# Kernel optimization log

Hardware: AMD Instinct MI355X
Metric: run time of the kernel (lower is better)

## Reference

```python
import jax, jax.numpy as jnp
import numpy as np
import math

B, T, IN_DIM = 2, 2048, 512
D, NH, MULT, N_LAYER = 512, 8, 4, 3
N = D * MULT // NH  # per-head latent dim = 256
OUT_DIM = 512
THETA = 2 ** 16


def get_freqs(n):
    t = jnp.arange(n, dtype=jnp.float32)
    q = jnp.floor(t / 2.0) * 2.0  # quantize(q=2)
    return 1.0 / (THETA ** (q / n)) / (2.0 * math.pi)


def ln(x, eps=1e-5):
    mu = jnp.mean(x, axis=-1, keepdims=True)
    var = jnp.var(x, axis=-1, keepdims=True)
    return (x - mu) * jax.lax.rsqrt(var + eps)


def rope(phases, v):
    # phases: [T, N] broadcastable to v [B, nh, T, N]
    p = (phases % 1.0) * (2.0 * math.pi)
    pc, ps = jnp.cos(p), jnp.sin(p)
    # interleave rotate: out[..., 2i] = -v[..., 2i+1], out[..., 2i+1] = v[..., 2i]
    v_rot = jnp.stack((-v[..., 1::2], v[..., ::2]), axis=-1).reshape(v.shape)
    return v * pc + v_rot * ps


def setup_inputs() -> dict:
    key = jax.random.key(0)
    ks = jax.random.split(key, 8)
    std = 0.02
    return {
        "x": jax.random.normal(ks[0], (B, T, IN_DIM), dtype=jnp.float32),
        "w_in": jax.random.normal(ks[1], (IN_DIM, D), dtype=jnp.float32) * std,
        "b_in": jnp.zeros((D,), dtype=jnp.float32),
        "encoder": jax.random.normal(ks[2], (NH, D, N), dtype=jnp.float32) * std,
        "encoder_v": jax.random.normal(ks[3], (NH, D, N), dtype=jnp.float32) * std,
        "decoder": jax.random.normal(ks[4], (NH * N, D), dtype=jnp.float32) * std,
        "head_w": jax.random.normal(ks[5], (D, OUT_DIM), dtype=jnp.float32) * std,
        "head_b": jnp.zeros((OUT_DIM,), dtype=jnp.float32),
    }


def reference(x, w_in, b_in, encoder, encoder_v, decoder, head_w, head_b):
    freqs = get_freqs(N)  # [N]
    t_idx = jnp.arange(T, dtype=jnp.float32)
    phases = t_idx[:, None] * freqs[None, :]  # [T, N]
    # strict lower-triangular causal mask (tril diagonal=-1)
    mask = (jnp.arange(T)[:, None] > jnp.arange(T)[None, :])  # [T, T]
    dec = decoder.reshape(NH, N, D)

    xs = ln(x @ w_in + b_in)  # [B, T, D]
    for _ in range(N_LAYER):
        x_res = xs
        x_sparse = jax.nn.relu(jnp.einsum('btd,hdn->bhtn', xs, encoder))  # [B,nh,T,N]
        QR = rope(phases, x_sparse)
        scores = jnp.einsum('bhtn,bhsn->bhts', QR, QR)
        scores = jnp.where(mask, scores, 0.0)
        yKV = jnp.einsum('bhts,bsd->bhtd', scores, xs)  # V = x (head-broadcast)
        yKV = ln(yKV)
        y_sparse = jax.nn.relu(jnp.einsum('bhtd,hdn->bhtn', yKV, encoder_v))
        xy_sparse = x_sparse * y_sparse  # dropout p=0 -> identity
        yMLP = jnp.einsum('bhtn,hnd->btd', xy_sparse, dec)
        xs = ln(x_res + ln(yMLP))
    logits = xs @ head_w + head_b
    return logits
```

## Files before the change

kernel.cpp:

```cpp
#include <hip/hip_runtime.h>
#include <math.h>

constexpr int B_  = 2;
constexpr int T_  = 2048;
constexpr int D_  = 512;
constexpr int NH_ = 8;
constexpr int NL_ = 256;
constexpr int HN_ = NH_ * NL_;
constexpr int BT_ = B_ * T_;

typedef __bf16 v8bf __attribute__((ext_vector_type(8)));
typedef float  v4f  __attribute__((ext_vector_type(4)));
typedef unsigned short us8 __attribute__((ext_vector_type(8)));
typedef unsigned short us4 __attribute__((ext_vector_type(4)));

__device__ inline unsigned short f2b(float f) {
    union { float f; unsigned u; } v{f};
    unsigned r = v.u + 0x7FFF + ((v.u >> 16) & 1);
    return (unsigned short)(r >> 16);
}
__device__ inline float b2f(unsigned short u) {
    union { unsigned u; float f; } v{(unsigned)u << 16};
    return v.f;
}

__device__ __forceinline__ void g2l16(const void* g, void* l) {
    __builtin_amdgcn_global_load_lds(
        (const __attribute__((address_space(1))) void*)g,
        (__attribute__((address_space(3))) void*)l, 16, 0, 0);
}

#define TILE_IDS                                              \
    int tid = threadIdx.x;                                    \
    int lane = tid & 63, wid = tid >> 6;                      \
    int wm = (wid & 1) * 64, wn = (wid >> 1) * 64;            \
    int ln16 = lane & 15, q = lane >> 4;                      \
    int srl = lane >> 2, scl = (lane & 3) * 8;                \
    (void)wm; (void)wn;

#define T128_STAGE(Ab, lda, Bb, ldb, k0, buf)                 \
    _Pragma("unroll")                                         \
    for (int ci = 0; ci < 4; ++ci) {                          \
        int c = wid * 4 + ci;                                 \
        if (c < 8) {                                          \
            int r = c * 16 + srl;                             \
            g2l16(Ab + (long)r * lda + (k0) + scl,            \
                  (char*)As[buf] + c * 1024);                 \
        } else {                                              \
            int r = (c - 8) * 16 + srl;                       \
            g2l16(Bb + (long)r * ldb + (k0) + scl,            \
                  (char*)Bs[buf] + (c - 8) * 1024);           \
        }                                                     \
    }

#define TILE_MFMA(Asx, Bsx)                                   \
    {                                                         \
        v8bf af[4], bfr[4];                                   \
        _Pragma("unroll")                                     \
        for (int r = 0; r < 4; ++r)                           \
            af[r] = *(const v8bf*)&Asx[wm + r * 16 + ln16][q * 8]; \
        _Pragma("unroll")                                     \
        for (int c = 0; c < 4; ++c)                           \
            bfr[c] = *(const v8bf*)&Bsx[wn + c * 16 + ln16][q * 8]; \
        _Pragma("unroll")                                     \
        for (int r = 0; r < 4; ++r)                           \
            _Pragma("unroll")                                 \
            for (int c = 0; c < 4; ++c)                       \
                acc[r][c] = __builtin_amdgcn_mfma_f32_16x16x32_bf16( \
                    af[r], bfr[c], acc[r][c], 0, 0, 0);       \
    }

template <int KS, bool RELU, bool MUL, bool BF16OUT>
__global__ __launch_bounds__(256) void gemm128(
    const unsigned short* __restrict__ A, int lda, long sA,
    const unsigned short* __restrict__ Bt, int ldb, long sB,
    void* __restrict__ Cv, int ldc, long sC,
    const unsigned short* __restrict__ mulp, int K) {
    constexpr int NHF = KS / 32;
    int m0 = blockIdx.y * 128, n0 = blockIdx.x * 128, z = blockIdx.z;
    __shared__ unsigned short As[2][NHF][128][32];
    __shared__ unsigned short Bs[2][NHF][128][32];
    const unsigned short* Ab = A  + (long)z * sA + (long)m0 * lda;
    const unsigned short* Bb = Bt + (long)z * sB + (long)n0 * ldb;
    TILE_IDS
    v4f acc[4][4] = {};
    auto stageK = [&](int k0, int buf) {
        #pragma unroll
        for (int h = 0; h < NHF; ++h)
            #pragma unroll
            for (int ci = 0; ci < 4; ++ci) {
                int c = wid * 4 + ci;
                if (c < 8)
                    g2l16(Ab + (long)(c * 16 + srl) * lda + k0 + h * 32 + scl,
                          (char*)As[buf][h] + c * 1024);
                else
                    g2l16(Bb + (long)((c - 8) * 16 + srl) * ldb + k0 + h * 32 +
                              scl,
                          (char*)Bs[buf][h] + (c - 8) * 1024);
            }
    };
    stageK(0, 0);
    __syncthreads();
    int cur = 0;
    for (int k0 = 0; k0 < K; k0 += KS) {
        if (k0 + KS < K) stageK(k0 + KS, cur ^ 1);
        #pragma unroll
        for (int h = 0; h < NHF; ++h)
            TILE_MFMA(As[cur][h], Bs[cur][h])
        __syncthreads();
        cur ^= 1;
    }
    float* Cf = (float*)Cv;
    unsigned short* Cb = (unsigned short*)Cv;
    long zoff = (long)z * sC;
    #pragma unroll
    for (int r = 0; r < 4; ++r)
        #pragma unroll
        for (int c = 0; c < 4; ++c)
            #pragma unroll
            for (int e = 0; e < 4; ++e) {
                int row = m0 + wm + r * 16 + q * 4 + e;
                int col = n0 + wn + c * 16 + ln16;
                float v = acc[r][c][e];
                if (RELU) v = fmaxf(v, 0.f);
                long idx = zoff + (long)row * ldc + col;
                if (MUL) v *= b2f(mulp[idx]);
                if (BF16OUT) Cb[idx] = f2b(v);
                else         Cf[idx] = v;
            }
}

__global__ __launch_bounds__(256) void enc_rope(
    const unsigned short* __restrict__ A,
    const unsigned short* __restrict__ Bt,
    unsigned short* __restrict__ xsp,
    unsigned short* __restrict__ qrh,
    unsigned short* __restrict__ qrT) {
    int m0 = blockIdx.y * 128, n0 = blockIdx.x * 128;
    __shared__ unsigned short As[2][2][128][32];
    __shared__ unsigned short Bs[2][2][128][32];
    unsigned short (*lt)[68] = (unsigned short(*)[68])&As[0][0][0][0];
    const unsigned short* Ab = A + (long)m0 * 512;
    const unsigned short* Bb = Bt + (long)n0 * 512;
    TILE_IDS
    v4f acc[4][4] = {};
    auto stageK = [&](int k0, int buf) {
        #pragma unroll
        for (int h = 0; h < 2; ++h)
            #pragma unroll
            for (int ci = 0; ci < 4; ++ci) {
                int c = wid * 4 + ci;
                if (c < 8)
                    g2l16(Ab + (long)(c * 16 + srl) * 512 + k0 + h * 32 + scl,
                          (char*)As[buf][h] + c * 1024);
                else
                    g2l16(Bb + (long)((c - 8) * 16 + srl) * 512 + k0 + h * 32 +
                              scl,
                          (char*)Bs[buf][h] + (c - 8) * 1024);
            }
    };
    stageK(0, 0);
    __syncthreads();
    int cur = 0;
    for (int k0 = 0; k0 < 512; k0 += 64) {
        if (k0 + 64 < 512) stageK(k0 + 64, cur ^ 1);
        TILE_MFMA(As[cur][0], Bs[cur][0])
        TILE_MFMA(As[cur][1], Bs[cur][1])
        __syncthreads();
        cur ^= 1;
    }
    int bb = m0 >> 11;
    int tbase = m0 & (T_ - 1);
    #pragma unroll
    for (int half = 0; half < 2; ++half) {
        if (wm == half * 64) {
            #pragma unroll
            for (int r = 0; r < 4; ++r)
                #pragma unroll
                for (int c = 0; c < 4; ++c)
                    #pragma unroll
                    for (int e = 0; e < 4; ++e) {
                        int rl = wm + r * 16 + q * 4 + e;
                        int col = n0 + wn + c * 16 + ln16;
                        float v = fmaxf(acc[r][c][e], 0.f);
                        xsp[(long)(m0 + rl) * HN_ + col] = f2b(v);
                        int n = col & (NL_ - 1);
                        int n2 = n >> 1;
                        float fr = exp2f(-(float)n2 * 0.125f) *
                                   (float)(1.0 / (2.0 * M_PI));
                        float ph = (float)(tbase + rl) * fr;
                        ph = (ph - floorf(ph)) * (float)(2.0 * M_PI);
                        float s, cc;
                        __sincosf(ph, &s, &cc);
                        float vp = __shfl_xor(v, 1, 64);
                        float o = (n & 1) ? (v * cc + vp * s)
                                          : (v * cc - vp * s);
                        int hh = col >> 8;
                        qrh[((long)(bb * 8 + hh) * T_ + tbase + rl) * NL_ + n] =
                            f2b(o);
                        lt[wn + c * 16 + ln16][rl & 63] = f2b(o);
                    }
        }
        __syncthreads();
        {
            int nrow = tid >> 1, tseg = (tid & 1) * 32;
            int colg = n0 + nrow;
            int hh = colg >> 8, nn = colg & (NL_ - 1);
            long ob = ((long)(bb * 8 + hh) * NL_ + nn) * T_ + tbase +
                      half * 64 + tseg;
            #pragma unroll
            for (int u = 0; u < 8; ++u)
                *(us4*)&qrT[ob + u * 4] = *(const us4*)&lt[nrow][tseg + u * 4];
        }
        __syncthreads();
    }
}

__global__ __launch_bounds__(256) void ct_gemm(
    const unsigned short* __restrict__ xsT,
    const unsigned short* __restrict__ qrT,
    unsigned short* __restrict__ Ct) {
    int z = blockIdx.x, nt = blockIdx.y;
    int j = blockIdx.z >> 2, mt = blockIdx.z & 3;
    int b = z >> 3;
    const unsigned short* Ab =
        xsT + (long)b * D_ * T_ + (long)(mt * 128) * T_ + j * 128;
    const unsigned short* Bb =
        qrT + (long)z * NL_ * T_ + (long)(nt * 128) * T_ + j * 128;
    __shared__ unsigned short As[2][128][32];
    __shared__ unsigned short Bs[2][128][32];
    TILE_IDS
    v4f acc[4][4] = {};
    T128_STAGE(Ab, T_, Bb, T_, 0, 0)
    __syncthreads();
    int cur = 0;
    for (int k0 = 0; k0 < 128; k0 += 32) {
        if (k0 + 32 < 128) { T128_STAGE(Ab, T_, Bb, T_, k0 + 32, cur ^ 1) }
        TILE_MFMA(As[cur], Bs[cur])
        __syncthreads();
        cur ^= 1;
    }
    unsigned short* ob = Ct + ((long)z * 16 + j) * 512 * 256;
    #pragma unroll
    for (int r = 0; r < 4; ++r)
        #pragma unroll
        for (int c = 0; c < 4; ++c)
            #pragma unroll
            for (int e = 0; e < 4; ++e) {
                int row = mt * 128 + wm + r * 16 + q * 4 + e;
                int col = nt * 128 + wn + c * 16 + ln16;
                ob[(long)row * 256 + col] = f2b(acc[r][c][e]);
            }
}

__global__ __launch_bounds__(256) void prefix_k(unsigned short* __restrict__ Ct) {
    int z = blockIdx.x, dg = blockIdx.y;
    int d = dg * 8 + (threadIdx.x >> 5);
    int n0 = (threadIdx.x & 31) * 8;
    long base = ((long)z * 16) * 512 * 256 + (long)d * 256 + n0;
    constexpr long S = 512 * 256;
    us8 vals[16];
    #pragma unroll
    for (int i = 0; i < 16; ++i)
        vals[i] = *(const us8*)&Ct[base + (long)i * S];
    float acc[8] = {};
    #pragma unroll
    for (int i = 0; i < 16; ++i) {
        us8 o;
        #pragma unroll
        for (int e = 0; e < 8; ++e) o[e] = f2b(acc[e]);
        *(us8*)&Ct[base + (long)i * S] = o;
        #pragma unroll
        for (int e = 0; e < 8; ++e) acc[e] += b2f(vals[i][e]);
    }
}

#define SD_STAGE(k0, buf)                                     \
    _Pragma("unroll")                                         \
    for (int ci = 0; ci < 2; ++ci) {                          \
        int c = wid * 2 + ci;                                 \
        g2l16(Ab + (long)(c * 16 + srl) * NL_ + (k0) + scl,   \
              (char*)As[buf] + c * 1024);                     \
    }

__global__ __launch_bounds__(256) void sdiag(const unsigned short* __restrict__ qr,
                                             unsigned short* __restrict__ Sd) {
    int z = blockIdx.x, i = blockIdx.y;
    const unsigned short* Ab = qr + ((long)z * T_ + i * 128) * NL_;
    __shared__ unsigned short As[2][128][32];
    TILE_IDS
    v4f acc[4][4] = {};
    SD_STAGE(0, 0)
    __syncthreads();
    int cur = 0;
    for (int k0 = 0; k0 < NL_; k0 += 32) {
        if (k0 + 32 < NL_) { SD_STAGE(k0 + 32, cur ^ 1) }
        TILE_MFMA(As[cur], As[cur])
        __syncthreads();
        cur ^= 1;
    }
    unsigned short* ob = Sd + ((long)z * 16 + i) * 16384;
    #pragma unroll
    for (int r = 0; r < 4; ++r)
        #pragma unroll
        for (int c = 0; c < 4; ++c)
            #pragma unroll
            for (int e = 0; e < 4; ++e) {
                int row = wm + r * 16 + q * 4 + e;
                int col = wn + c * 16 + ln16;
                float v = acc[r][c][e];
                if (row <= col) v = 0.f;
                ob[row * 128 + col] = f2b(v);
            }
}

__global__ __launch_bounds__(256) void pxg(
    const unsigned short* __restrict__ qr,
    const unsigned short* __restrict__ Pt,
    const unsigned short* __restrict__ Sd,
    const unsigned short* __restrict__ xsT,
    unsigned short* __restrict__ ykvu,
    float* __restrict__ part) {
    int z = blockIdx.x, i = blockIdx.y, nt = blockIdx.z;
    int b = z >> 3, h = z & 7;
    int n0 = nt * 128;
    const unsigned short* A1 = qr + ((long)z * T_ + i * 128) * NL_;
    const unsigned short* B1 =
        Pt + ((long)z * 16 + i) * 512 * 256 + (long)n0 * 256;
    const unsigned short* A2 = Sd + ((long)z * 16 + i) * 16384;
    const unsigned short* B2 =
        xsT + (long)b * D_ * T_ + (long)n0 * T_ + i * 128;
    __shared__ unsigned short As[2][128][32];
    __shared__ unsigned short Bs[2][128][32];
    __shared__ float sred[128][2][2];
    TILE_IDS
    v4f acc[4][4] = {};
    auto stage = [&](int s) {
        const unsigned short* Ap;
        const unsigned short* Bp;
        long lda, ldb;
        int k0;
        if (s < 8) { Ap = A1; lda = NL_; Bp = B1; ldb = 256; k0 = s * 32; }
        else       { Ap = A2; lda = 128; Bp = B2; ldb = T_;  k0 = (s - 8) * 32; }
        int bi = s & 1;
        #pragma unroll
        for (int ci = 0; ci < 4; ++ci) {
            int c = wid * 4 + ci;
            if (c < 8)
                g2l16(Ap + (long)(c * 16 + srl) * lda + k0 + scl,
                      (char*)As[bi] + c * 1024);
            else
                g2l16(Bp + (long)((c - 8) * 16 + srl) * ldb + k0 + scl,
                      (char*)Bs[bi] + (c - 8) * 1024);
        }
    };
    stage(0);
    __syncthreads();
    for (int s = 0; s < 12; ++s) {
        if (s < 11) stage(s + 1);
        int bi = s & 1;
        TILE_MFMA(As[bi], Bs[bi])
        __syncthreads();
    }
    long obase = ((long)h * BT_ + (long)b * T_ + i * 128) * D_ + n0;
    #pragma unroll
    for (int r = 0; r < 4; ++r) {
        float s1[4] = {}, s2[4] = {};
        #pragma unroll
        for (int c = 0; c < 4; ++c)
            #pragma unroll
            for (int e = 0; e < 4; ++e) {
                float v = acc[r][c][e];
                s1[e] += v;
                s2[e] += v * v;
                int rl = wm + r * 16 + q * 4 + e;
                int col = wn + c * 16 + ln16;
                ykvu[obase + (long)rl * D_ + col] = f2b(v);
            }
        #pragma unroll
        for (int e = 0; e < 4; ++e) {
            #pragma unroll
            for (int off = 1; off < 16; off <<= 1) {
                s1[e] += __shfl_xor(s1[e], off, 64);
                s2[e] += __shfl_xor(s2[e], off, 64);
            }
            if (ln16 == 0) {
                int rl = wm + r * 16 + q * 4 + e;
                sred[rl][wid >> 1][0] = s1[e];
                sred[rl][wid >> 1][1] = s2[e];
            }
        }
    }
    __syncthreads();
    if (tid < 128) {
        float a = sred[tid][0][0] + sred[tid][1][0];
        float sq = sred[tid][0][1] + sred[tid][1][1];
        long pb = ((((long)z * 16 + i) * 4 + nt) * 128 + tid) * 2;
        part[pb] = a;
        part[pb + 1] = sq;
    }
}

__global__ __launch_bounds__(256) void lnykv(unsigned short* __restrict__ ykv,
                                             const float* __restrict__ part) {
    int tid = threadIdx.x;
    int lane = tid & 63, wid = tid >> 6;
    long row = (long)blockIdx.x * 4 + wid;
    int h = (int)(row >> 12), bt = (int)row & 4095;
    int b = bt >> 11, t = bt & 2047;
    int z = b * 8 + h, i = t >> 7, tl = t & 127;
    long pb = ((((long)z * 16 + i) * 4) * 128 + tl) * 2;
    float s1 = part[pb] + part[pb + 256] + part[pb + 512] + part[pb + 768];
    float s2 = part[pb + 1] + part[pb + 257] + part[pb + 513] + part[pb + 769];
    float mu = s1 * (1.0f / 512.0f);
    float var = s2 * (1.0f / 512.0f) - mu * mu;
    float inv = rsqrtf(var + 1e-5f);
    long ib = row * 512 + lane * 8;
    us8 v = *(const us8*)&ykv[ib];
    us8 o;
    #pragma unroll
    for (int e = 0; e < 8; ++e) o[e] = f2b((b2f(v[e]) - mu) * inv);
    *(us8*)&ykv[ib] = o;
}

__global__ __launch_bounds__(256) void trans_cast(
    const float* __restrict__ in, long sIn, unsigned short* __restrict__ out,
    long sOut, int R, int Cc) {
    __shared__ float tl[32][33];
    int z = blockIdx.z;
    int r0 = blockIdx.y * 32, c0 = blockIdx.x * 32;
    int tx = threadIdx.x & 31, ty = threadIdx.x >> 5;
    const float* ip = in + (long)z * sIn;
    unsigned short* op = out + (long)z * sOut;
    #pragma unroll
    for (int j = 0; j < 4; ++j)
        tl[ty + j * 8][tx] = ip[(long)(r0 + ty + j * 8) * Cc + c0 + tx];
    __syncthreads();
    #pragma unroll
    for (int j = 0; j < 4; ++j)
        op[(long)(c0 + ty + j * 8) * R + r0 + tx] = f2b(tl[tx][ty + j * 8]);
}

__global__ __launch_bounds__(256) void cast_b(const float* __restrict__ in,
                                              unsigned short* __restrict__ out) {
    long i = ((long)blockIdx.x * 256 + threadIdx.x) * 4;
    float4 v = *(const float4*)&in[i];
    ushort4 o;
    o.x = f2b(v.x); o.y = f2b(v.y); o.z = f2b(v.z); o.w = f2b(v.w);
    *(ushort4*)&out[i] = o;
}

__global__ __launch_bounds__(256) void add_out4(const float* __restrict__ t,
                                                long slice,
                                                const float* __restrict__ bias,
                                                float* __restrict__ o) {
    long i = ((long)blockIdx.x * 256 + threadIdx.x) * 4;
    float4 v0 = *(const float4*)&t[i];
    float4 v1 = *(const float4*)&t[i + slice];
    float4 v2 = *(const float4*)&t[i + 2 * slice];
    float4 v3 = *(const float4*)&t[i + 3 * slice];
    float4 bv = *(const float4*)&bias[i & 511];
    float4 r;
    r.x = v0.x + v1.x + v2.x + v3.x + bv.x;
    r.y = v0.y + v1.y + v2.y + v3.y + bv.y;
    r.z = v0.z + v1.z + v2.z + v3.z + bv.z;
    r.w = v0.w + v1.w + v2.w + v3.w + bv.w;
    *(float4*)&o[i] = r;
}

__device__ inline float2 block_reduce2(float a, float b) {
    __shared__ float sa[4], sb[4];
    #pragma unroll
    for (int off = 32; off; off >>= 1) {
        a += __shfl_down(a, off, 64);
        b += __shfl_down(b, off, 64);
    }
    __syncthreads();
    int w = threadIdx.x >> 6;
    if ((threadIdx.x & 63) == 0) { sa[w] = a; sb[w] = b; }
    __syncthreads();
    return make_float2(sa[0] + sa[1] + sa[2] + sa[3],
                       sb[0] + sb[1] + sb[2] + sb[3]);
}
__device__ inline float2 ln_pair(float2 v) {
    float2 s = block_reduce2(v.x + v.y, 0.f);
    float mu = s.x * (1.0f / 512.0f);
    float dx = v.x - mu, dy = v.y - mu;
    float2 q = block_reduce2(dx * dx + dy * dy, 0.f);
    float inv = rsqrtf(q.x * (1.0f / 512.0f) + 1e-5f);
    return make_float2(dx * inv, dy * inv);
}

__global__ __launch_bounds__(256) void ln_dual4(const float* __restrict__ t,
                                                long slice,
                                                const float* __restrict__ bias,
                                                float* __restrict__ outf,
                                                unsigned short* __restrict__ outb) {
    long row = blockIdx.x;
    int c = threadIdx.x * 2;
    long i = row * 512 + c;
    float2 v0 = *(const float2*)&t[i];
    float2 v1 = *(const float2*)&t[i + slice];
    float2 v2 = *(const float2*)&t[i + 2 * slice];
    float2 v3 = *(const float2*)&t[i + 3 * slice];
    float2 bv = *(const float2*)&bias[c];
    float2 v = make_float2(v0.x + v1.x + v2.x + v3.x + bv.x,
                           v0.y + v1.y + v2.y + v3.y + bv.y);
    float2 o = ln_pair(v);
    *(float2*)&outf[i] = o;
    ushort2 ob; ob.x = f2b(o.x); ob.y = f2b(o.y);
    *(ushort2*)&outb[i] = ob;
}

__global__ __launch_bounds__(256) void combine_dual4(
    const float* __restrict__ t, long slice, const float* __restrict__ xres,
    float* __restrict__ outf, unsigned short* __restrict__ outb) {
    long row = blockIdx.x;
    int c = threadIdx.x * 2;
    long i = row * 512 + c;
    float2 v0 = *(const float2*)&t[i];
    float2 v1 = *(const float2*)&t[i + slice];
    float2 v2 = *(const float2*)&t[i + 2 * slice];
    float2 v3 = *(const float2*)&t[i + 3 * slice];
    float2 y = make_float2(v0.x + v1.x + v2.x + v3.x,
                           v0.y + v1.y + v2.y + v3.y);
    float2 l = ln_pair(y);
    float2 r = *(const float2*)&xres[i];
    float2 z = make_float2(r.x + l.x, r.y + l.y);
    float2 o = ln_pair(z);
    *(float2*)&outf[i] = o;
    ushort2 ob; ob.x = f2b(o.x); ob.y = f2b(o.y);
    *(ushort2*)&outb[i] = ob;
}

extern "C" void kernel_launch(void* const* d_in, const int* in_sizes, int n_in,
                              void* d_out, int out_size, void* d_ws,
                              size_t ws_size, hipStream_t stream) {
    const float* x      = (const float*)d_in[0];
    const float* w_in   = (const float*)d_in[1];
    const float* b_in   = (const float*)d_in[2];
    const float* enc    = (const float*)d_in[3];
    const float* enc_v  = (const float*)d_in[4];
    const float* dec    = (const float*)d_in[5];
    const float* head_w = (const float*)d_in[6];
    const float* head_b = (const float*)d_in[7];
    float* out = (float*)d_out;

    char* w = (char*)d_ws;
    auto alloc = [&](size_t bytes) { void* p = (void*)w; w += bytes; return p; };
    unsigned short* w_inT = (unsigned short*)alloc((size_t)512 * 512 * 2);
    unsigned short* headT = (unsigned short*)alloc((size_t)512 * 512 * 2);
    unsigned short* encT  = (unsigned short*)alloc((size_t)NH_ * NL_ * D_ * 2);
    unsigned short* encvT = (unsigned short*)alloc((size_t)NH_ * NL_ * D_ * 2);
    unsigned short* decT  = (unsigned short*)alloc((size_t)D_ * HN_ * 2);
    unsigned short* xb    = (unsigned short*)alloc((size_t)BT_ * D_ * 2);
    float*          tmp   = (float*)alloc((size_t)4 * BT_ * D_ * 4);
    float*          xsf0  = (float*)alloc((size_t)BT_ * D_ * 4);
    float*          xsf1  = (float*)alloc((size_t)BT_ * D_ * 4);
    unsigned short* xs_b  = (unsigned short*)alloc((size_t)BT_ * D_ * 2);
    unsigned short* xsT   = (unsigned short*)alloc((size_t)B_ * D_ * T_ * 2);
    unsigned short* xsp   = (unsigned short*)alloc((size_t)BT_ * HN_ * 2);
    unsigned short* qrh   = (unsigned short*)alloc((size_t)BT_ * HN_ * 2);
    unsigned short* qrT   = (unsigned short*)alloc((size_t)BT_ * HN_ * 2);
    unsigned short* Ct    = (unsigned short*)alloc((size_t)256 * 512 * 256 * 2);
    unsigned short* Sd    = (unsigned short*)alloc((size_t)256 * 128 * 128 * 2);
    unsigned short* ykv   = (unsigned short*)alloc((size_t)NH_ * BT_ * D_ * 2);
    float*          part  = (float*)alloc((size_t)256 * 4 * 128 * 2 * 4);
    const long SL = (long)BT_ * D_;

    cast_b<<<BT_ * D_ / 1024, 256, 0, stream>>>(x, xb);
    trans_cast<<<dim3(16, 16, 1), 256, 0, stream>>>(w_in, 0, w_inT, 0, 512, 512);
    trans_cast<<<dim3(16, 16, 1), 256, 0, stream>>>(head_w, 0, headT, 0, 512, 512);
    trans_cast<<<dim3(8, 16, 8), 256, 0, stream>>>(enc, (long)D_ * NL_, encT,
                                                   (long)NL_ * D_, D_, NL_);
    trans_cast<<<dim3(8, 16, 8), 256, 0, stream>>>(enc_v, (long)D_ * NL_, encvT,
                                                   (long)NL_ * D_, D_, NL_);
    trans_cast<<<dim3(16, 64, 1), 256, 0, stream>>>(dec, 0, decT, 0, HN_, D_);

    gemm128<64, false, false, false>
        <<<dim3(4, 32, 4), 256, 0, stream>>>(xb, D_, 128, w_inT, D_, 128, tmp,
                                             D_, SL, nullptr, 128);
    ln_dual4<<<BT_, 256, 0, stream>>>(tmp, SL, b_in, xsf0, xs_b);
    trans_cast<<<dim3(16, 64, 2), 256, 0, stream>>>(xsf0, (long)T_ * D_, xsT,
                                                    (long)D_ * T_, T_, D_);

    float* xin = xsf0;
    float* xout = xsf1;
    for (int l = 0; l < 3; ++l) {
        enc_rope<<<dim3(16, 32), 256, 0, stream>>>(xs_b, encT, xsp, qrh, qrT);
        ct_gemm<<<dim3(16, 2, 64), 256, 0, stream>>>(xsT, qrT, Ct);
        prefix_k<<<dim3(16, 64), 256, 0, stream>>>(Ct);
        sdiag<<<dim3(16, 16), 256, 0, stream>>>(qrh, Sd);
        pxg<<<dim3(16, 16, 4), 256, 0, stream>>>(qrh, Ct, Sd, xsT, ykv, part);
        lnykv<<<NH_ * BT_ / 4, 256, 0, stream>>>(ykv, part);
        gemm128<64, true, true, true>
            <<<dim3(2, 32, 8), 256, 0, stream>>>(
                ykv, D_, (long)BT_ * D_, encvT, D_, (long)NL_ * D_, xsp, HN_,
                NL_, xsp, 512);
        gemm128<64, false, false, false>
            <<<dim3(4, 32, 4), 256, 0, stream>>>(
                xsp, HN_, 512, decT, HN_, 512, tmp, D_, SL, nullptr, 512);
        combine_dual4<<<BT_, 256, 0, stream>>>(tmp, SL, xin, xout, xs_b);
        trans_cast<<<dim3(16, 64, 2), 256, 0, stream>>>(xout, (long)T_ * D_,
                                                        xsT, (long)D_ * T_, T_,
                                                        D_);
        float* t = xin; xin = xout; xout = t;
    }

    gemm128<64, false, false, false>
        <<<dim3(4, 32, 4), 256, 0, stream>>>(xs_b, D_, 128, headT, D_, 128, tmp,
                                             D_, SL, nullptr, 128);
    add_out4<<<BT_ * 512 / 1024, 256, 0, stream>>>(tmp, SL, head_b, out);
}
```

Baseline: 655.0 us.

## Fold yKV layernorm into encoder_v GEMM epilogue via column sums

```diff
diff --git a/kernel.cpp b/kernel.cpp
--- a/kernel.cpp
+++ b/kernel.cpp
@@ -70,12 +70,13 @@
                     af[r], bfr[c], acc[r][c], 0, 0, 0);       \
     }
 
-template <int KS, bool RELU, bool MUL, bool BF16OUT>
+template <int KS, bool RELU, bool MUL, bool BF16OUT, bool LNA>
 __global__ __launch_bounds__(256) void gemm128(
     const unsigned short* __restrict__ A, int lda, long sA,
     const unsigned short* __restrict__ Bt, int ldb, long sB,
     void* __restrict__ Cv, int ldc, long sC,
-    const unsigned short* __restrict__ mulp, int K) {
+    const unsigned short* __restrict__ mulp, int K,
+    const float* __restrict__ muinv, const float* __restrict__ colsum) {
     constexpr int NHF = KS / 32;
     int m0 = blockIdx.y * 128, n0 = blockIdx.x * 128, z = blockIdx.z;
     __shared__ unsigned short As[2][NHF][128][32];
@@ -122,6 +123,11 @@
                 int row = m0 + wm + r * 16 + q * 4 + e;
                 int col = n0 + wn + c * 16 + ln16;
                 float v = acc[r][c][e];
+                if (LNA) {
+                    float2 mi = *(const float2*)&muinv[((long)z * BT_ + row) * 2];
+                    float cs = colsum[(long)z * NL_ + col];
+                    v = mi.y * (v - mi.x * cs);
+                }
                 if (RELU) v = fmaxf(v, 0.f);
                 long idx = zoff + (long)row * ldc + col;
                 if (MUL) v *= b2f(mulp[idx]);
@@ -401,26 +407,32 @@
     }
 }
 
-__global__ __launch_bounds__(256) void lnykv(unsigned short* __restrict__ ykv,
-                                             const float* __restrict__ part) {
-    int tid = threadIdx.x;
-    int lane = tid & 63, wid = tid >> 6;
-    long row = (long)blockIdx.x * 4 + wid;
-    int h = (int)(row >> 12), bt = (int)row & 4095;
-    int b = bt >> 11, t = bt & 2047;
-    int z = b * 8 + h, i = t >> 7, tl = t & 127;
-    long pb = ((((long)z * 16 + i) * 4) * 128 + tl) * 2;
+__global__ __launch_bounds__(128) void lnstats(const float* __restrict__ part,
+                                               float* __restrict__ muinv) {
+    int z = blockIdx.x, i = blockIdx.y, t = threadIdx.x;
+    long pb = ((((long)z * 16 + i) * 4) * 128 + t) * 2;
     float s1 = part[pb] + part[pb + 256] + part[pb + 512] + part[pb + 768];
     float s2 = part[pb + 1] + part[pb + 257] + part[pb + 513] + part[pb + 769];
     float mu = s1 * (1.0f / 512.0f);
     float var = s2 * (1.0f / 512.0f) - mu * mu;
     float inv = rsqrtf(var + 1e-5f);
-    long ib = row * 512 + lane * 8;
-    us8 v = *(const us8*)&ykv[ib];
-    us8 o;
-    #pragma unroll
-    for (int e = 0; e < 8; ++e) o[e] = f2b((b2f(v[e]) - mu) * inv);
-    *(us8*)&ykv[ib] = o;
+    int b = z >> 3, h = z & 7;
+    long row = (long)h * BT_ + (long)b * T_ + i * 128 + t;
+    muinv[row * 2]     = mu;
+    muinv[row * 2 + 1] = inv;
+}
+
+__global__ __launch_bounds__(256) void colsum_k(
+    const unsigned short* __restrict__ encvT, float* __restrict__ cs) {
+    int lane = threadIdx.x & 63, wv = threadIdx.x >> 6;
+    int g = blockIdx.x * 4 + wv;
+    us8 v = *(const us8*)&encvT[(long)g * 512 + lane * 8];
+    float s = 0.f;
+    #pragma unroll
+    for (int e = 0; e < 8; ++e) s += b2f(v[e]);
+    #pragma unroll
+    for (int off = 1; off < 64; off <<= 1) s += __shfl_xor(s, off, 64);
+    if (lane == 0) cs[g] = s;
 }
 
 __global__ __launch_bounds__(256) void trans_cast(
@@ -566,6 +578,8 @@
     unsigned short* Sd    = (unsigned short*)alloc((size_t)256 * 128 * 128 * 2);
     unsigned short* ykv   = (unsigned short*)alloc((size_t)NH_ * BT_ * D_ * 2);
     float*          part  = (float*)alloc((size_t)256 * 4 * 128 * 2 * 4);
+    float*          muinv = (float*)alloc((size_t)NH_ * BT_ * 2 * 4);
+    float*          csum  = (float*)alloc((size_t)HN_ * 4);
     const long SL = (long)BT_ * D_;
 
     cast_b<<<BT_ * D_ / 1024, 256, 0, stream>>>(x, xb);
@@ -576,10 +590,12 @@
     trans_cast<<<dim3(8, 16, 8), 256, 0, stream>>>(enc_v, (long)D_ * NL_, encvT,
                                                    (long)NL_ * D_, D_, NL_);
     trans_cast<<<dim3(16, 64, 1), 256, 0, stream>>>(dec, 0, decT, 0, HN_, D_);
-
-    gemm128<64, false, false, false>
+    colsum_k<<<HN_ / 4, 256, 0, stream>>>(encvT, csum);
+
+    gemm128<64, false, false, false, false>
         <<<dim3(4, 32, 4), 256, 0, stream>>>(xb, D_, 128, w_inT, D_, 128, tmp,
-                                             D_, SL, nullptr, 128);
+                                             D_, SL, nullptr, 128, nullptr,
+                                             nullptr);
     ln_dual4<<<BT_, 256, 0, stream>>>(tmp, SL, b_in, xsf0, xs_b);
     trans_cast<<<dim3(16, 64, 2), 256, 0, stream>>>(xsf0, (long)T_ * D_, xsT,
                                                     (long)D_ * T_, T_, D_);
@@ -592,14 +608,15 @@
         prefix_k<<<dim3(16, 64), 256, 0, stream>>>(Ct);
         sdiag<<<dim3(16, 16), 256, 0, stream>>>(qrh, Sd);
         pxg<<<dim3(16, 16, 4), 256, 0, stream>>>(qrh, Ct, Sd, xsT, ykv, part);
-        lnykv<<<NH_ * BT_ / 4, 256, 0, stream>>>(ykv, part);
-        gemm128<64, true, true, true>
+        lnstats<<<dim3(16, 16), 128, 0, stream>>>(part, muinv);
+        gemm128<64, true, true, true, true>
             <<<dim3(2, 32, 8), 256, 0, stream>>>(
                 ykv, D_, (long)BT_ * D_, encvT, D_, (long)NL_ * D_, xsp, HN_,
-                NL_, xsp, 512);
-        gemm128<64, false, false, false>
+                NL_, xsp, 512, muinv, csum);
+        gemm128<64, false, false, false, false>
             <<<dim3(4, 32, 4), 256, 0, stream>>>(
-                xsp, HN_, 512, decT, HN_, 512, tmp, D_, SL, nullptr, 512);
+                xsp, HN_, 512, decT, HN_, 512, tmp, D_, SL, nullptr, 512,
+                nullptr, nullptr);
         combine_dual4<<<BT_, 256, 0, stream>>>(tmp, SL, xin, xout, xs_b);
         trans_cast<<<dim3(16, 64, 2), 256, 0, stream>>>(xout, (long)T_ * D_,
                                                         xsT, (long)D_ * T_, T_,
@@ -607,8 +624,9 @@
         float* t = xin; xin = xout; xout = t;
     }
 
-    gemm128<64, false, false, false>
+    gemm128<64, false, false, false, false>
         <<<dim3(4, 32, 4), 256, 0, stream>>>(xs_b, D_, 128, headT, D_, 128, tmp,
-                                             D_, SL, nullptr, 128);
+                                             D_, SL, nullptr, 128, nullptr,
+                                             nullptr);
     add_out4<<<BT_ * 512 / 1024, 256, 0, stream>>>(tmp, SL, head_b, out);
 }
```

Result: faster. 627.5 us (-4.2%).
